# Performance work log

Measured on AMD Instinct MI355X. Metric: run time of the kernel, lower is better.

The kernel has to match this reference:

```python
import jax, jax.numpy as jnp
import numpy as np

TEMPERATURE = 1.0          # max(args.matching_temperature=1.0, 1e-6)
CONSISTENCY_WEIGHT = 0.5   # max(args.matching_consistency_weight=0.5, 0.0)
EPS = 1e-6

N, M, D, K = 16384, 16384, 128, 5


def setup_inputs() -> dict:
    key = jax.random.key(0)
    k1, k2, k3 = jax.random.split(key, 3)
    query = jax.random.normal(k1, (N, D), dtype=jnp.float32)
    memory_bank = jax.random.normal(k2, (M, D), dtype=jnp.float32)
    # per-memory-entry neighbor scale (positive), as in _build_patch_library_statistics
    neighbor_scale_bank = jax.random.uniform(k3, (M,), dtype=jnp.float32) + 0.1
    return {"query": query, "memory_bank": memory_bank,
            "neighbor_scale_bank": neighbor_scale_bank, "k": K}


def reference(query, memory_bank, neighbor_scale_bank, k):
    # Euclidean cdist: [N, M]
    q2 = jnp.sum(query * query, axis=-1, keepdims=True)            # [N,1]
    m2 = jnp.sum(memory_bank * memory_bank, axis=-1)               # [M]
    d2 = q2 + m2 - 2.0 * (query @ memory_bank.T)                   # [N,M]
    dist = jnp.sqrt(jnp.maximum(d2, 1e-12))

    # torch.topk(largest=False) -> k smallest distances, ascending
    neg_d, knn_indices = jax.lax.top_k(-dist, k)                   # [N,k]
    knn_distances = -neg_d

    # adaptive_knn reduction (_reduce_knn_distances)
    weights = jax.nn.softmax(-knn_distances / TEMPERATURE, axis=1)
    weighted_distance = jnp.sum(weights * knn_distances, axis=1)   # [N]

    neighbor_scale = jnp.mean(neighbor_scale_bank[knn_indices], axis=1)  # [N]
    normalized_distance = weighted_distance / jnp.maximum(neighbor_scale, EPS)

    mean_d = jnp.mean(knn_distances, axis=1)
    std_d = jnp.sqrt(jnp.maximum(
        jnp.mean((knn_distances - mean_d[:, None]) ** 2, axis=1), 0.0))  # unbiased=False
    consistency = std_d / jnp.maximum(mean_d, EPS)

    return normalized_distance * (1.0 + CONSISTENCY_WEIGHT * consistency)
```

## Files before the change

### kernel.cpp

```cpp
#include <hip/hip_runtime.h>
#include <hip/hip_bf16.h>
#include <math.h>

#define N_Q 16384
#define N_M 16384
#define DIM 128
#define KNN 5
#define SPLITS 8
#define COLS_PER_SPLIT (N_M / SPLITS)
#define ITERS (COLS_PER_SPLIT / 128)
#define BROWS 256
#define TSEL 8
#define TSEL2 16
#define LLIST 4
#define BIGF 3.0e38f

typedef __bf16 bf16x8 __attribute__((ext_vector_type(8)));
typedef float f32x4 __attribute__((ext_vector_type(4)));

__device__ __forceinline__ void gl2lds16(const void* g, void* l) {
    __builtin_amdgcn_global_load_lds(
        (const __attribute__((address_space(1))) void*)g,
        (__attribute__((address_space(3))) void*)l, 16, 0, 0);
}

__device__ __forceinline__ unsigned umed3(unsigned a, unsigned b, unsigned c) {
    unsigned d;
    asm("v_med3_u32 %0, %1, %2, %3" : "=v"(d) : "v"(a), "v"(b), "v"(c));
    return d;
}

template <int D>
__device__ __forceinline__ void insD(unsigned (&L)[D], unsigned k) {
#pragma unroll
    for (int i = D - 1; i >= 1; --i) L[i] = umed3(L[i - 1], L[i], k);
    L[0] = min(L[0], k);
}

__global__ void prep_kernel(const float* __restrict__ q,
                            const float* __restrict__ mem,
                            float* __restrict__ q2, float* __restrict__ m2,
                            float* __restrict__ m2b,
                            __hip_bfloat16* __restrict__ qb,
                            __hip_bfloat16* __restrict__ mb) {
    int gt = blockIdx.x * blockDim.x + threadIdx.x;
    int wid = gt >> 6;
    int lane = gt & 63;
    bool isq = wid < N_Q;
    int r = isq ? wid : wid - N_Q;
    const float* src = (isq ? q : mem) + (size_t)r * DIM;
    __hip_bfloat16* bdst = (isq ? qb : mb) + (size_t)r * DIM;
    float2 v = reinterpret_cast<const float2*>(src)[lane];
    float sc = isq ? 1.0f : -2.0f;
    __hip_bfloat162 bv;
    bv.x = __float2bfloat16(sc * v.x);
    bv.y = __float2bfloat16(sc * v.y);
    reinterpret_cast<__hip_bfloat162*>(bdst)[lane] = bv;
    float s = fmaf(v.x, v.x, v.y * v.y);
#pragma unroll
    for (int off = 32; off > 0; off >>= 1) s += __shfl_down(s, off, 64);
    if (lane == 0) {
        if (isq) {
            q2[r] = s;
        } else {
            m2[r] = s;
            m2b[r] = s + 256.0f;
        }
    }
}

__global__ __launch_bounds__(256, 2) void knn_tops_kernel(
    const __hip_bfloat16* __restrict__ qb, const __hip_bfloat16* __restrict__ mb,
    const float* __restrict__ m2b, unsigned* __restrict__ candK) {
    __shared__ __align__(16) unsigned char smem[33792];
    const int tid = threadIdx.x;
    const int w = tid >> 6;
    const int lane = tid & 63;
    const int i16 = lane & 15;
    const int g = lane >> 4;
    const int row0 = blockIdx.x * BROWS;
    const int col0 = blockIdx.y * COLS_PER_SPLIT;

    bf16x8 afrag[4][4];
#pragma unroll
    for (int ti = 0; ti < 4; ++ti) {
        const __hip_bfloat16* qrow =
            qb + (size_t)(row0 + w * 64 + ti * 16 + i16) * DIM;
#pragma unroll
        for (int ks = 0; ks < 4; ++ks)
            afrag[ti][ks] = *reinterpret_cast<const bf16x8*>(qrow + ks * 32 + g * 8);
    }

    unsigned lst[16][LLIST];
#pragma unroll
    for (int rr = 0; rr < 16; ++rr)
#pragma unroll
        for (int j = 0; j < LLIST; ++j) lst[rr][j] = 0xFFFFFFFFu;

    const int lds_base = i16 * 256 + ((g ^ (i16 & 7)) << 4);
    int soff[8];
#pragma unroll
    for (int it = 0; it < 8; ++it) {
        int fg = w * 512 + it * 64 + lane;
        int c = fg >> 4, sg = fg & 15;
        int gk = (sg & 8) | ((sg ^ c) & 7);
        soff[it] = c * DIM + gk * 8;
    }
    const __hip_bfloat16* mbt = mb + (size_t)col0 * DIM;

    for (int t = 0; t < ITERS; ++t) {
        __syncthreads();
#pragma unroll
        for (int it = 0; it < 8; ++it)
            gl2lds16(mbt + soff[it], smem + w * 8192 + it * 1024);
        mbt += 128 * DIM;
        __syncthreads();

        float m2r[8];
        unsigned colv[8];
#pragma unroll
        for (int h = 0; h < 2; ++h)
#pragma unroll
            for (int c = 0; c < 4; ++c) {
                int cl = col0 + t * 128 + h * 64 + c * 16 + i16;
                m2r[h * 4 + c] = m2b[cl];
                colv[h * 4 + c] = (unsigned)cl;
            }
#pragma unroll
        for (int half = 0; half < 2; ++half) {
#pragma unroll
            for (int cc = 0; cc < 2; ++cc) {
                f32x4 acc[4][2];
#pragma unroll
                for (int ti = 0; ti < 4; ++ti)
#pragma unroll
                    for (int c2 = 0; c2 < 2; ++c2) {
                        float m = m2r[half * 4 + cc * 2 + c2];
                        acc[ti][c2] = (f32x4){m, m, m, m};
                    }
#pragma unroll
                for (int ks = 0; ks < 4; ++ks) {
                    const unsigned char* bp =
                        smem + (lds_base ^ (ks << 6)) + half * 16384;
#pragma unroll
                    for (int c2 = 0; c2 < 2; ++c2) {
                        int ct = cc * 2 + c2;
                        bf16x8 bfr =
                            *reinterpret_cast<const bf16x8*>(bp + ct * 4096);
#pragma unroll
                        for (int ti = 0; ti < 4; ++ti)
                            acc[ti][c2] = __builtin_amdgcn_mfma_f32_16x16x32_bf16(
                                afrag[ti][ks], bfr, acc[ti][c2], 0, 0, 0);
                    }
                }
#pragma unroll
                for (int ti = 0; ti < 4; ++ti) {
#pragma unroll
                    for (int r = 0; r < 4; ++r) {
                        const int rr = ti * 4 + r;
#pragma unroll
                        for (int c2 = 0; c2 < 2; ++c2) {
                            unsigned k = (__float_as_uint(acc[ti][c2][r]) &
                                          0xFFFFC000u) |
                                         colv[half * 4 + cc * 2 + c2];
                            insD(lst[rr], k);
                        }
                    }
                }
            }
        }
    }

    __syncthreads();

#pragma unroll
    for (int rr = 0; rr < 16; ++rr) {
        unsigned pv[LLIST];
#pragma unroll
        for (int j = 0; j < LLIST; ++j)
            pv[j] = (unsigned)__shfl_xor((int)lst[rr][j], 8, 64);
#pragma unroll
        for (int j = 0; j < LLIST; ++j) insD(lst[rr], pv[j]);
    }
    unsigned* MG = (unsigned*)smem;
    if (i16 < 8) {
#pragma unroll
        for (int rr = 0; rr < 16; ++rr) {
            int row = w * 64 + (rr >> 2) * 16 + g * 4 + (rr & 3);
#pragma unroll
            for (int j = 0; j < LLIST; ++j)
                MG[row * 33 + i16 * LLIST + j] = lst[rr][j];
        }
    }
    __syncthreads();
    {
        unsigned bk[TSEL];
#pragma unroll
        for (int j = 0; j < TSEL; ++j) bk[j] = 0xFFFFFFFFu;
        for (int c = 0; c < 32; ++c) {
            unsigned k = MG[tid * 33 + c];
            insD(bk, k);
        }
        size_t base = (size_t)(row0 + tid) * (SPLITS * TSEL) + blockIdx.y * TSEL;
        *reinterpret_cast<uint4*>(candK + base) =
            make_uint4(bk[0], bk[1], bk[2], bk[3]);
        *reinterpret_cast<uint4*>(candK + base + 4) =
            make_uint4(bk[4], bk[5], bk[6], bk[7]);
    }
}

__global__ void merge_kernel(const unsigned* __restrict__ candK,
                             int* __restrict__ candI2) {
    int row = blockIdx.x * blockDim.x + threadIdx.x;
    const unsigned* ck = candK + (size_t)row * (SPLITS * TSEL);
    unsigned v[TSEL2];
#pragma unroll
    for (int j = 0; j < TSEL2; ++j) v[j] = 0xFFFFFFFFu;
    for (int s4 = 0; s4 < 16; ++s4) {
        uint4 kk = reinterpret_cast<const uint4*>(ck)[s4];
        insD(v, kk.x);
        insD(v, kk.y);
        insD(v, kk.z);
        insD(v, kk.w);
    }
#pragma unroll
    for (int j = 0; j < TSEL2; ++j)
        candI2[(size_t)row * TSEL2 + j] = (int)(v[j] & 0x3FFFu);
}

__global__ __launch_bounds__(256) void finalize_kernel(
    const float* __restrict__ q, const float* __restrict__ mem,
    const float* __restrict__ q2, const float* __restrict__ m2,
    const int* __restrict__ candI2, const float* __restrict__ scaleb,
    float* __restrict__ out) {
    int wv = threadIdx.x >> 6, lane = threadIdx.x & 63;
    int n = blockIdx.x * 4 + wv;
    int cand = lane >> 2, qd = lane & 3;
    int ci = candI2[(size_t)n * TSEL2 + cand];
    const float4* qr = reinterpret_cast<const float4*>(q + (size_t)n * DIM) + qd * 8;
    const float4* mr = reinterpret_cast<const float4*>(mem + (size_t)ci * DIM) + qd * 8;
    float dot = 0.f;
#pragma unroll
    for (int k = 0; k < 8; ++k) {
        float4 a = qr[k], b = mr[k];
        dot = fmaf(a.x, b.x, fmaf(a.y, b.y, fmaf(a.z, b.z, fmaf(a.w, b.w, dot))));
    }
    dot += __shfl_xor(dot, 1, 64);
    dot += __shfl_xor(dot, 2, 64);
    float v = (qd == 0) ? (q2[n] + m2[ci] - 2.f * dot) : BIGF;

    float dk[KNN]; int ik[KNN];
#pragma unroll
    for (int r = 0; r < KNN; ++r) {
        float mv = v; int ml = lane;
#pragma unroll
        for (int off = 32; off > 0; off >>= 1) {
            float ov = __shfl_xor(mv, off, 64);
            int   ol = __shfl_xor(ml, off, 64);
            if (ov < mv || (ov == mv && ol < ml)) { mv = ov; ml = ol; }
        }
        dk[r] = sqrtf(fmaxf(mv, 1e-12f));
        ik[r] = __shfl(ci, ml, 64);
        if (lane == ml) v = BIGF;
    }
    if (lane == 0) {
        float dmin = dk[0];
        float se = 0.f, wd = 0.f, sm = 0.f, ssc = 0.f;
#pragma unroll
        for (int j = 0; j < KNN; ++j) {
            float e = expf(-(dk[j] - dmin));
            se += e;
            wd = fmaf(e, dk[j], wd);
            sm += dk[j];
            ssc += scaleb[ik[j]];
        }
        wd /= se;
        float scale = ssc * 0.2f;
        float nd = wd / fmaxf(scale, 1e-6f);
        float mean = sm * 0.2f;
        float var = 0.f;
#pragma unroll
        for (int j = 0; j < KNN; ++j) {
            float dd = dk[j] - mean;
            var = fmaf(dd, dd, var);
        }
        var *= 0.2f;
        float cons = sqrtf(var) / fmaxf(mean, 1e-6f);
        out[n] = nd * (1.f + 0.5f * cons);
    }
}

extern "C" void kernel_launch(void* const* d_in, const int* in_sizes, int n_in,
                              void* d_out, int out_size, void* d_ws,
                              size_t ws_size, hipStream_t stream) {
    const float* query  = (const float*)d_in[0];
    const float* mem    = (const float*)d_in[1];
    const float* scaleb = (const float*)d_in[2];
    float* out = (float*)d_out;

    float* q2 = (float*)d_ws;
    float* m2 = q2 + N_Q;
    float* m2b = m2 + N_M;
    __hip_bfloat16* qb = (__hip_bfloat16*)(m2b + N_M);
    __hip_bfloat16* mb = qb + (size_t)N_Q * DIM;
    unsigned* candK = (unsigned*)(mb + (size_t)N_M * DIM);
    int* candI2 = (int*)(candK + (size_t)N_Q * SPLITS * TSEL);

    prep_kernel<<<(N_Q + N_M) / 4, 256, 0, stream>>>(query, mem, q2, m2, m2b,
                                                     qb, mb);
    dim3 gridB(N_Q / BROWS, SPLITS);
    knn_tops_kernel<<<gridB, 256, 0, stream>>>(qb, mb, m2b, candK);
    merge_kernel<<<N_Q / 256, 256, 0, stream>>>(candK, candI2);
    finalize_kernel<<<N_Q / 4, 256, 0, stream>>>(query, mem, q2, m2, candI2,
                                                 scaleb, out);
}
```

Measured before the change: 200.8 us.

## Double-buffer memory tiles in LDS with smaller tiles, more splits and occupancy

The main kernel now loads the memory-bank tile for the next iteration into a second LDS buffer while it computes on the current one. This needs only one barrier per iteration instead of a load-then-wait pattern. Tiles shrink from 128 to 64 columns, the column dimension is split 16 ways instead of 8, and launch bounds now ask for 4 blocks per CU. The aim is to hide global-to-LDS latency and raise parallelism. The costs are more register pressure and possible spills from the tighter launch bound, and twice as many partial candidates for the merge kernel to process.

```diff
diff --git a/kernel.cpp b/kernel.cpp
--- a/kernel.cpp
+++ b/kernel.cpp
@@ -6,9 +6,10 @@
 #define N_M 16384
 #define DIM 128
 #define KNN 5
-#define SPLITS 8
+#define SPLITS 16
 #define COLS_PER_SPLIT (N_M / SPLITS)
-#define ITERS (COLS_PER_SPLIT / 128)
+#define TILE_COLS 64
+#define ITERS (COLS_PER_SPLIT / TILE_COLS)
 #define BROWS 256
 #define TSEL 8
 #define TSEL2 16
@@ -69,7 +70,7 @@
     }
 }
 
-__global__ __launch_bounds__(256, 2) void knn_tops_kernel(
+__global__ __launch_bounds__(256, 4) void knn_tops_kernel(
     const __hip_bfloat16* __restrict__ qb, const __hip_bfloat16* __restrict__ mb,
     const float* __restrict__ m2b, unsigned* __restrict__ candK) {
     __shared__ __align__(16) unsigned char smem[33792];
@@ -98,76 +99,77 @@
         for (int j = 0; j < LLIST; ++j) lst[rr][j] = 0xFFFFFFFFu;
 
     const int lds_base = i16 * 256 + ((g ^ (i16 & 7)) << 4);
-    int soff[8];
-#pragma unroll
-    for (int it = 0; it < 8; ++it) {
-        int fg = w * 512 + it * 64 + lane;
+    int soff[4];
+#pragma unroll
+    for (int it = 0; it < 4; ++it) {
+        int fg = w * 256 + it * 64 + lane;
         int c = fg >> 4, sg = fg & 15;
         int gk = (sg & 8) | ((sg ^ c) & 7);
         soff[it] = c * DIM + gk * 8;
     }
     const __hip_bfloat16* mbt = mb + (size_t)col0 * DIM;
 
+#pragma unroll
+    for (int it = 0; it < 4; ++it)
+        gl2lds16(mbt + soff[it], smem + w * 4096 + it * 1024);
+    mbt += TILE_COLS * DIM;
+
     for (int t = 0; t < ITERS; ++t) {
         __syncthreads();
-#pragma unroll
-        for (int it = 0; it < 8; ++it)
-            gl2lds16(mbt + soff[it], smem + w * 8192 + it * 1024);
-        mbt += 128 * DIM;
-        __syncthreads();
-
-        float m2r[8];
-        unsigned colv[8];
-#pragma unroll
-        for (int h = 0; h < 2; ++h)
-#pragma unroll
-            for (int c = 0; c < 4; ++c) {
-                int cl = col0 + t * 128 + h * 64 + c * 16 + i16;
-                m2r[h * 4 + c] = m2b[cl];
-                colv[h * 4 + c] = (unsigned)cl;
+        const unsigned char* cbuf = smem + ((t & 1) << 14);
+        if (t + 1 < ITERS) {
+            unsigned char* nbuf = smem + (((t + 1) & 1) << 14);
+#pragma unroll
+            for (int it = 0; it < 4; ++it)
+                gl2lds16(mbt + soff[it], nbuf + w * 4096 + it * 1024);
+            mbt += TILE_COLS * DIM;
+        }
+
+        float m2r[4];
+        unsigned colv[4];
+#pragma unroll
+        for (int cg = 0; cg < 4; ++cg) {
+            int cl = col0 + t * TILE_COLS + cg * 16 + i16;
+            m2r[cg] = m2b[cl];
+            colv[cg] = (unsigned)cl;
+        }
+
+#pragma unroll
+        for (int c = 0; c < 2; ++c) {
+            f32x4 acc[4][2];
+#pragma unroll
+            for (int ti = 0; ti < 4; ++ti)
+#pragma unroll
+                for (int c2 = 0; c2 < 2; ++c2) {
+                    float m = m2r[c * 2 + c2];
+                    acc[ti][c2] = (f32x4){m, m, m, m};
+                }
+#pragma unroll
+            for (int ks = 0; ks < 4; ++ks) {
+                const unsigned char* bp = cbuf + (lds_base ^ (ks << 6));
+#pragma unroll
+                for (int c2 = 0; c2 < 2; ++c2) {
+                    bf16x8 bfr = *reinterpret_cast<const bf16x8*>(
+                        bp + (c * 2 + c2) * 4096);
+#pragma unroll
+                    for (int ti = 0; ti < 4; ++ti)
+                        acc[ti][c2] = __builtin_amdgcn_mfma_f32_16x16x32_bf16(
+                            afrag[ti][ks], bfr, acc[ti][c2], 0, 0, 0);
+                }
             }
 #pragma unroll
-        for (int half = 0; half < 2; ++half) {
-#pragma unroll
-            for (int cc = 0; cc < 2; ++cc) {
-                f32x4 acc[4][2];
-#pragma unroll
-                for (int ti = 0; ti < 4; ++ti)
+            for (int ti = 0; ti < 4; ++ti)
+#pragma unroll
+                for (int r = 0; r < 4; ++r) {
+                    const int rr = ti * 4 + r;
 #pragma unroll
                     for (int c2 = 0; c2 < 2; ++c2) {
-                        float m = m2r[half * 4 + cc * 2 + c2];
-                        acc[ti][c2] = (f32x4){m, m, m, m};
-                    }
-#pragma unroll
-                for (int ks = 0; ks < 4; ++ks) {
-                    const unsigned char* bp =
-                        smem + (lds_base ^ (ks << 6)) + half * 16384;
-#pragma unroll
-                    for (int c2 = 0; c2 < 2; ++c2) {
-                        int ct = cc * 2 + c2;
-                        bf16x8 bfr =
-                            *reinterpret_cast<const bf16x8*>(bp + ct * 4096);
-#pragma unroll
-                        for (int ti = 0; ti < 4; ++ti)
-                            acc[ti][c2] = __builtin_amdgcn_mfma_f32_16x16x32_bf16(
-                                afrag[ti][ks], bfr, acc[ti][c2], 0, 0, 0);
+                        unsigned k = (__float_as_uint(acc[ti][c2][r]) &
+                                      0xFFFFC000u) |
+                                     colv[c * 2 + c2];
+                        insD(lst[rr], k);
                     }
                 }
-#pragma unroll
-                for (int ti = 0; ti < 4; ++ti) {
-#pragma unroll
-                    for (int r = 0; r < 4; ++r) {
-                        const int rr = ti * 4 + r;
-#pragma unroll
-                        for (int c2 = 0; c2 < 2; ++c2) {
-                            unsigned k = (__float_as_uint(acc[ti][c2][r]) &
-                                          0xFFFFC000u) |
-                                         colv[half * 4 + cc * 2 + c2];
-                            insD(lst[rr], k);
-                        }
-                    }
-                }
-            }
         }
     }
 
@@ -216,7 +218,7 @@
     unsigned v[TSEL2];
 #pragma unroll
     for (int j = 0; j < TSEL2; ++j) v[j] = 0xFFFFFFFFu;
-    for (int s4 = 0; s4 < 16; ++s4) {
+    for (int s4 = 0; s4 < (SPLITS * TSEL) / 4; ++s4) {
         uint4 kk = reinterpret_cast<const uint4*>(ck)[s4];
         insD(v, kk.x);
         insD(v, kk.y);
```

After: 662.1 us. 230% more time.
